# Optimization experiments

Measured on AMD Instinct MI355X. Metric: run time of the kernel, lower is better.

## Reference

```python
import jax, jax.numpy as jnp
import numpy as np
from jax import lax

B, C, H, W, K = 32, 128, 56, 56, 5
CR = C // 4          # reduced channels in weight-gen MLP
CE = 4 * C           # expanded channels
EPS = 1e-6


def setup_inputs() -> dict:
    key = jax.random.key(0)
    ks = jax.random.split(key, 8)
    s = lambda fan: 1.0 / np.sqrt(fan)
    return {
        "x": jax.random.normal(ks[0], (B, C, H, W), jnp.float32),
        "w_fc1": jax.random.normal(ks[1], (CR, C), jnp.float32) * s(C),
        "ln1_w": jnp.ones((CR,), jnp.float32),
        "ln1_b": jnp.zeros((CR,), jnp.float32),
        "w_fc2": jax.random.normal(ks[2], (C * K * K, CR), jnp.float32) * s(CR),
        "ln2_w": jnp.ones((C,), jnp.float32),
        "ln2_b": jnp.zeros((C,), jnp.float32),
        "w_expand": jax.random.normal(ks[3], (CE, C), jnp.float32) * s(C),
        "w_shrink": jax.random.normal(ks[4], (C, CE), jnp.float32) * s(CE),
        "grn_gamma": jax.random.normal(ks[5], (CE,), jnp.float32) * 0.1,
        "grn_beta": jax.random.normal(ks[6], (CE,), jnp.float32) * 0.1,
    }


def _ln(v, w, b, axis):
    u = v.mean(axis, keepdims=True)
    s2 = jnp.square(v - u).mean(axis, keepdims=True)
    return (v - u) * lax.rsqrt(s2 + EPS) * w + b


def reference(x, w_fc1, ln1_w, ln1_b, w_fc2, ln2_w, ln2_b, w_expand, w_shrink,
              grn_gamma, grn_beta):
    b, c, h, w = x.shape
    # ---- dynamic weight generation: pool -> fc1 -> LN -> fc2 ----
    pooled = x.mean((2, 3))                                  # [B, C]
    hdn = pooled @ w_fc1.T                                   # [B, CR]
    hdn = _ln(hdn, ln1_w, ln1_b, axis=-1)                    # channels_first LN over CR
    dyn = hdn @ w_fc2.T                                      # [B, C*K*K]
    dyn_w = dyn.reshape(b * c, 1, K, K)                      # per-sample depthwise kernels
    # ---- per-sample dynamic depthwise conv (groups = B*C) ----
    pad = K // 2
    out = lax.conv_general_dilated(
        x.reshape(1, b * c, h, w), dyn_w,
        window_strides=(1, 1), padding=[(pad, pad), (pad, pad)],
        dimension_numbers=("NCHW", "OIHW", "NCHW"),
        feature_group_count=b * c,
    ).reshape(b, c, h, w)
    # ---- LN (channels_first) over channel dim ----
    u = out.mean(1, keepdims=True)
    s2 = jnp.square(out - u).mean(1, keepdims=True)
    out = (out - u) * lax.rsqrt(s2 + EPS)
    out = ln2_w[None, :, None, None] * out + ln2_b[None, :, None, None]
    # ---- expand 1x1 -> GELU -> GRN -> shrink 1x1 ----
    out = jnp.einsum("bchw,oc->bohw", out, w_expand)         # [B, 4C, H, W]
    out = jax.nn.gelu(out, approximate=False)
    gx = jnp.sqrt(jnp.sum(jnp.square(out), axis=(2, 3), keepdims=True))  # [B,4C,1,1]
    nx = gx / (gx.mean(1, keepdims=True) + EPS)
    g = grn_gamma[None, :, None, None]
    bt = grn_beta[None, :, None, None]
    out = g * (out * nx) + bt + out
    out = jnp.einsum("bohw,co->bchw", out, w_shrink)         # [B, C, H, W]
    return out + x
```

## Files before the change

### kernel.cpp

```cpp
#include <hip/hip_runtime.h>
#include <hip/hip_bf16.h>

#define B_   32
#define C_   128
#define H_   56
#define W_   56
#define HW_  (H_*W_)
#define BHW_ (B_*HW_)
#define K5_  5
#define KK_  25
#define CR_  32
#define CE_  512
#define EPS_ 1e-6f

typedef __hip_bfloat16 bf16;
typedef __attribute__((ext_vector_type(8))) short short8;
typedef __attribute__((ext_vector_type(4))) float f32x4;


__device__ __forceinline__ float wave_reduce_sum(float v) {
#pragma unroll
  for (int off = 32; off > 0; off >>= 1) v += __shfl_down(v, off, 64);
  return v;
}
__device__ __forceinline__ float bf2f(unsigned short u) {
  return __uint_as_float(((unsigned)u) << 16);
}
__device__ __forceinline__ unsigned short f2bf_bits(float f) {
  bf16 h = __float2bfloat16(f);
  unsigned short u;
  __builtin_memcpy(&u, &h, 2);
  return u;
}
__device__ __forceinline__ float fast_gelu(float v) {
  float t = __expf(-1.702f * v);
  return v * __builtin_amdgcn_rcpf(1.0f + t);
}

__global__ __launch_bounds__(256) void prep_kernel(const float* __restrict__ we,
                                                   const float* __restrict__ ws,
                                                   bf16* __restrict__ weB,
                                                   bf16* __restrict__ wsB,
                                                   float* __restrict__ gx2) {
  int i = blockIdx.x * 256 + threadIdx.x;
  if (i < CE_ * C_)          weB[i] = __float2bfloat16(we[i]);
  else if (i < 2 * CE_ * C_) wsB[i - CE_ * C_] = __float2bfloat16(ws[i - CE_ * C_]);
  else                       gx2[i - 2 * CE_ * C_] = 0.f;
}

__global__ __launch_bounds__(256) void pool_kernel(const float* __restrict__ x,
                                                   float* __restrict__ pooled) {
  int bc = blockIdx.x;
  const float4* xp4 = reinterpret_cast<const float4*>(x + (size_t)bc * HW_);
  float s = 0.f;
  for (int i = threadIdx.x; i < 784; i += 256) {
    float4 v = xp4[i];
    s += (v.x + v.y) + (v.z + v.w);
  }
  s = wave_reduce_sum(s);
  __shared__ float red[4];
  int lane = threadIdx.x & 63, wid = threadIdx.x >> 6;
  if (lane == 0) red[wid] = s;
  __syncthreads();
  if (threadIdx.x == 0) pooled[bc] = (red[0] + red[1] + red[2] + red[3]) * (1.0f / HW_);
}

__global__ __launch_bounds__(256) void fc_kernel(const float* __restrict__ pooled,
                                                 const float* __restrict__ w_fc1,
                                                 const float* __restrict__ ln1_w,
                                                 const float* __restrict__ ln1_b,
                                                 const float* __restrict__ w_fc2,
                                                 float* __restrict__ dyn) {
  int b = blockIdx.x;
  int tid = threadIdx.x;
  __shared__ float sp[C_];
  __shared__ float sh[CR_];
  __shared__ float shn[CR_];
  __shared__ float stats[2];
  if (tid < C_) sp[tid] = pooled[b * C_ + tid];
  __syncthreads();
  if (tid < CR_) {
    float acc = 0.f;
    const float* wr = w_fc1 + tid * C_;
#pragma unroll 4
    for (int c = 0; c < C_; ++c) acc += sp[c] * wr[c];
    sh[tid] = acc;
  }
  __syncthreads();
  if (tid == 0) {
    float u = 0.f;
    for (int j = 0; j < CR_; ++j) u += sh[j];
    u *= (1.0f / CR_);
    float v = 0.f;
    for (int j = 0; j < CR_; ++j) { float d = sh[j] - u; v += d * d; }
    v *= (1.0f / CR_);
    stats[0] = u;
    stats[1] = rsqrtf(v + EPS_);
  }
  __syncthreads();
  if (tid < CR_) shn[tid] = (sh[tid] - stats[0]) * stats[1] * ln1_w[tid] + ln1_b[tid];
  __syncthreads();
  for (int i = tid; i < C_ * KK_; i += 256) {
    const float* wr = w_fc2 + i * CR_;
    float acc = 0.f;
#pragma unroll
    for (int j = 0; j < CR_; ++j) acc += shn[j] * wr[j];
    dyn[b * (C_ * KK_) + i] = acc;
  }
}

__global__ __launch_bounds__(256) void conv_kernel(const float* __restrict__ x,
                                                   const float* __restrict__ dyn,
                                                   bf16* __restrict__ z) {
  int bc = blockIdx.x;
  int b = bc >> 7;
  int c = bc & 127;
  int tid = threadIdx.x;
  __shared__ float xs[(H_ + 4) * 64];
  __shared__ float wks[KK_];
  {
    int r = tid >> 6;
    int rr = (r < 2) ? r : (56 + r);
    xs[rr * 64 + (tid & 63)] = 0.f;
  }
  if (tid < 224) {
    int r = tid >> 2, q = tid & 3;
    int col = (q < 2) ? q : (56 + q);
    xs[(r + 2) * 64 + col] = 0.f;
  }
  if (tid < KK_) wks[tid] = dyn[b * (C_ * KK_) + c * KK_ + tid];
  const float4* xp4 = reinterpret_cast<const float4*>(x + (size_t)bc * HW_);
  for (int i = tid; i < 784; i += 256) {
    float4 v = xp4[i];
    int h = i / 14, w4 = (i % 14) * 4;
    float* dst = &xs[(h + 2) * 64 + 2 + w4];
    dst[0] = v.x; dst[1] = v.y; dst[2] = v.z; dst[3] = v.w;
  }
  __syncthreads();
  float wr[KK_];
#pragma unroll
  for (int j = 0; j < KK_; ++j) wr[j] = wks[j];
  for (int g = tid; g < 784; g += 256) {
    int h = g / 14;
    int w4 = (g % 14) * 4;
    float a0 = 0.f, a1 = 0.f, a2 = 0.f, a3 = 0.f;
#pragma unroll
    for (int dh = 0; dh < K5_; ++dh) {
      const float* row = &xs[(h + dh) * 64 + w4];
      float4 va = *reinterpret_cast<const float4*>(row);
      float4 vb = *reinterpret_cast<const float4*>(row + 4);
      float v0 = va.x, v1 = va.y, v2 = va.z, v3 = va.w;
      float v4 = vb.x, v5 = vb.y, v6 = vb.z, v7 = vb.w;
      float u0 = wr[dh * 5 + 0], u1 = wr[dh * 5 + 1], u2 = wr[dh * 5 + 2];
      float u3 = wr[dh * 5 + 3], u4 = wr[dh * 5 + 4];
      a0 += v0 * u0 + v1 * u1 + v2 * u2 + v3 * u3 + v4 * u4;
      a1 += v1 * u0 + v2 * u1 + v3 * u2 + v4 * u3 + v5 * u4;
      a2 += v2 * u0 + v3 * u1 + v4 * u2 + v5 * u3 + v6 * u4;
      a3 += v3 * u0 + v4 * u1 + v5 * u2 + v6 * u3 + v7 * u4;
    }
    size_t base = (size_t)bc * HW_ + h * W_ + w4;
    ushort4 pk = make_ushort4(f2bf_bits(a0), f2bf_bits(a1), f2bf_bits(a2), f2bf_bits(a3));
    *reinterpret_cast<ushort4*>(reinterpret_cast<unsigned short*>(z) + base) = pk;
  }
}

__global__ __launch_bounds__(256) void ln_kernel(const bf16* __restrict__ z,
                                                 const float* __restrict__ ln2_w,
                                                 const float* __restrict__ ln2_b,
                                                 bf16* __restrict__ yT) {
  int hw0 = blockIdx.x * 64;
  int b = blockIdx.y;
  int tid = threadIdx.x;
  int wq = tid & 63;
  int cq = tid >> 6;
  __shared__ unsigned short zt[C_][64];
  __shared__ unsigned short yt[64][136];
  __shared__ float redS[4][64];
  __shared__ float redQ[4][64];
  __shared__ float meanArr[64];
  __shared__ float invArr[64];
  float s = 0.f, q = 0.f;
  const unsigned short* zp = reinterpret_cast<const unsigned short*>(z);
#pragma unroll 4
  for (int k = 0; k < 32; ++k) {
    int c = cq * 32 + k;
    unsigned short u = zp[((size_t)(b * C_ + c)) * HW_ + hw0 + wq];
    float v = bf2f(u);
    s += v;
    q += v * v;
    zt[c][wq] = u;
  }
  redS[cq][wq] = s;
  redQ[cq][wq] = q;
  __syncthreads();
  if (cq == 0) {
    float ss = redS[0][wq] + redS[1][wq] + redS[2][wq] + redS[3][wq];
    float qq = redQ[0][wq] + redQ[1][wq] + redQ[2][wq] + redQ[3][wq];
    float m = ss * (1.0f / C_);
    float var = qq * (1.0f / C_) - m * m;
    meanArr[wq] = m;
    invArr[wq] = rsqrtf(fmaxf(var, 0.f) + EPS_);
  }
  __syncthreads();
  float m = meanArr[wq], iv = invArr[wq];
#pragma unroll
  for (int g = 0; g < 4; ++g) {
    unsigned short pk[8];
#pragma unroll
    for (int i = 0; i < 8; ++i) {
      int c = cq * 32 + g * 8 + i;
      float v = bf2f(zt[c][wq]);
      pk[i] = f2bf_bits((v - m) * iv * ln2_w[c] + ln2_b[c]);
    }
    int4 t;
    __builtin_memcpy(&t, pk, 16);
    *reinterpret_cast<int4*>(&yt[wq][cq * 32 + g * 8]) = t;
  }
  __syncthreads();
  unsigned short* yp = reinterpret_cast<unsigned short*>(yT);
#pragma unroll
  for (int i = 0; i < 4; ++i) {
    int t = tid + 256 * i;
    int row = t >> 4, ch = t & 15;
    int4 v = *reinterpret_cast<const int4*>(&yt[row][ch * 8]);
    *reinterpret_cast<int4*>(yp + ((size_t)(b * HW_ + hw0 + row)) * C_ + ch * 8) = v;
  }
}

__global__ __launch_bounds__(256, 2) void expand_mfma(const bf16* __restrict__ yT,
                                                      const bf16* __restrict__ weB,
                                                      bf16* __restrict__ eT,
                                                      float* __restrict__ gx2) {
  int j0 = blockIdx.x * 128;
  int o0 = blockIdx.y * 128;
  int tid = threadIdx.x;
  int lane = tid & 63, wid = tid >> 6;
  int wm = wid >> 1, wn = wid & 1;
  int quad = lane >> 4, l15 = lane & 15;
  __shared__ __align__(16) char smem[2 * 128 * 136 * 2];
  short (*As)[136] = reinterpret_cast<short(*)[136]>(smem);
  short (*Bs)[136] = reinterpret_cast<short(*)[136]>(smem + 34816);
  const short* yS = reinterpret_cast<const short*>(yT);
  const short* weS = reinterpret_cast<const short*>(weB);
#pragma unroll
  for (int i = 0; i < 8; ++i) {
    int t = tid + 256 * i;
    int row = t >> 4, ch = t & 15;
    *reinterpret_cast<int4*>(&As[row][ch * 8]) =
        *reinterpret_cast<const int4*>(yS + (size_t)(j0 + row) * C_ + ch * 8);
    *reinterpret_cast<int4*>(&Bs[row][ch * 8]) =
        *reinterpret_cast<const int4*>(weS + (size_t)(o0 + row) * C_ + ch * 8);
  }
  __syncthreads();
  f32x4 acc[4][4] = {};
#pragma unroll
  for (int ks = 0; ks < 4; ++ks) {
    short8 a[4], b[4];
#pragma unroll
    for (int mf = 0; mf < 4; ++mf)
      a[mf] = *reinterpret_cast<const short8*>(&As[wm * 64 + mf * 16 + l15][ks * 32 + quad * 8]);
#pragma unroll
    for (int nf = 0; nf < 4; ++nf)
      b[nf] = *reinterpret_cast<const short8*>(&Bs[wn * 64 + nf * 16 + l15][ks * 32 + quad * 8]);
#pragma unroll
    for (int mf = 0; mf < 4; ++mf)
#pragma unroll
      for (int nf = 0; nf < 4; ++nf)
        acc[mf][nf] = __builtin_amdgcn_mfma_f32_16x16x32_bf16(a[mf], b[nf], acc[mf][nf], 0, 0, 0);
  }
  __syncthreads();
  short (*Es)[136] = reinterpret_cast<short(*)[136]>(smem);
#pragma unroll
  for (int mf = 0; mf < 4; ++mf) {
    int jm = j0 + wm * 64 + mf * 16;
    int bb = jm / HW_;
    int jrow = wm * 64 + mf * 16 + quad * 4;
#pragma unroll
    for (int nf = 0; nf < 4; ++nf) {
      int ocl = wn * 64 + nf * 16 + l15;
      float g2 = 0.f;
#pragma unroll
      for (int r = 0; r < 4; ++r) {
        float ge = fast_gelu(acc[mf][nf][r]);
        g2 += ge * ge;
        Es[jrow + r][ocl] = (short)f2bf_bits(ge);
      }
      g2 += __shfl_xor(g2, 16, 64);
      g2 += __shfl_xor(g2, 32, 64);
      if (quad == 0) atomicAdd(&gx2[bb * CE_ + o0 + ocl], g2);
    }
  }
  __syncthreads();
  unsigned short* eP = reinterpret_cast<unsigned short*>(eT);
#pragma unroll
  for (int i = 0; i < 8; ++i) {
    int t = tid + 256 * i;
    int row = t >> 4, ch = t & 15;
    int4 v = *reinterpret_cast<const int4*>(&Es[row][ch * 8]);
    *reinterpret_cast<int4*>(eP + (size_t)(j0 + row) * CE_ + o0 + ch * 8) = v;
  }
}

__global__ __launch_bounds__(512) void grn_scale_kernel(const float* __restrict__ gx2,
                                                        const float* __restrict__ gamma,
                                                        float* __restrict__ scale) {
  int b = blockIdx.x;
  int o = threadIdx.x;
  float gx = sqrtf(gx2[b * CE_ + o]);
  float s = wave_reduce_sum(gx);
  __shared__ float red[8];
  __shared__ float meansh;
  int lane = o & 63, wid = o >> 6;
  if (lane == 0) red[wid] = s;
  __syncthreads();
  if (o == 0) {
    float t = 0.f;
    for (int i = 0; i < 8; ++i) t += red[i];
    meansh = t * (1.0f / CE_);
  }
  __syncthreads();
  scale[b * CE_ + o] = 1.0f + gamma[o] * (gx / (meansh + EPS_));
}

__global__ __launch_bounds__(256) void sb_kernel(const float* __restrict__ w_shrink,
                                                 const float* __restrict__ beta,
                                                 float* __restrict__ sb) {
  int c = blockIdx.x;
  const float* wp = w_shrink + (size_t)c * CE_;
  float acc = 0.f;
  for (int o = threadIdx.x; o < CE_; o += 256) acc += wp[o] * beta[o];
  acc = wave_reduce_sum(acc);
  __shared__ float red[4];
  int lane = threadIdx.x & 63, wid = threadIdx.x >> 6;
  if (lane == 0) red[wid] = acc;
  __syncthreads();
  if (threadIdx.x == 0) sb[c] = red[0] + red[1] + red[2] + red[3];
}

__global__ __launch_bounds__(256, 2) void shrink_mfma(const bf16* __restrict__ eT,
                                                      const bf16* __restrict__ wsB,
                                                      const float* __restrict__ scale,
                                                      const float* __restrict__ sb,
                                                      const float* __restrict__ x,
                                                      float* __restrict__ out) {
  int hw0 = blockIdx.x * 128;
  int b = blockIdx.y;
  int tid = threadIdx.x;
  int lane = tid & 63, wid = tid >> 6;
  int wm = wid >> 1, wn = wid & 1;
  int quad = lane >> 4, l15 = lane & 15;
  __shared__ __align__(16) char smem[2 * 128 * 136 * 2];
  short (*As)[136] = reinterpret_cast<short(*)[136]>(smem);
  short (*Bs)[136] = reinterpret_cast<short(*)[136]>(smem + 34816);
  const short* eS  = reinterpret_cast<const short*>(eT) + (size_t)b * HW_ * CE_;
  const short* wsS = reinterpret_cast<const short*>(wsB);
  const float* scp = scale + b * CE_;
  f32x4 acc[4][4] = {};
#pragma unroll 1
  for (int kc = 0; kc < 4; ++kc) {
    int k0 = kc * 128;
#pragma unroll
    for (int i = 0; i < 8; ++i) {
      int t = tid + 256 * i;
      int row = t >> 4, ch = t & 15;
      int hwc = hw0 + row; if (hwc >= HW_) hwc = HW_ - 1;
      *reinterpret_cast<int4*>(&As[row][ch * 8]) =
          *reinterpret_cast<const int4*>(eS + (size_t)hwc * CE_ + k0 + ch * 8);
      int4 wv = *reinterpret_cast<const int4*>(wsS + (size_t)row * CE_ + k0 + ch * 8);
      float4 s0 = *reinterpret_cast<const float4*>(scp + k0 + ch * 8);
      float4 s1 = *reinterpret_cast<const float4*>(scp + k0 + ch * 8 + 4);
      unsigned short wu[8];
      __builtin_memcpy(wu, &wv, 16);
      unsigned short ru[8];
      ru[0] = f2bf_bits(bf2f(wu[0]) * s0.x);
      ru[1] = f2bf_bits(bf2f(wu[1]) * s0.y);
      ru[2] = f2bf_bits(bf2f(wu[2]) * s0.z);
      ru[3] = f2bf_bits(bf2f(wu[3]) * s0.w);
      ru[4] = f2bf_bits(bf2f(wu[4]) * s1.x);
      ru[5] = f2bf_bits(bf2f(wu[5]) * s1.y);
      ru[6] = f2bf_bits(bf2f(wu[6]) * s1.z);
      ru[7] = f2bf_bits(bf2f(wu[7]) * s1.w);
      int4 rv;
      __builtin_memcpy(&rv, ru, 16);
      *reinterpret_cast<int4*>(&Bs[row][ch * 8]) = rv;
    }
    __syncthreads();
#pragma unroll
    for (int ks = 0; ks < 4; ++ks) {
      short8 a[4], bfr[4];
#pragma unroll
      for (int mf = 0; mf < 4; ++mf)
        a[mf] = *reinterpret_cast<const short8*>(&As[wm * 64 + mf * 16 + l15][ks * 32 + quad * 8]);
#pragma unroll
      for (int nf = 0; nf < 4; ++nf)
        bfr[nf] = *reinterpret_cast<const short8*>(&Bs[wn * 64 + nf * 16 + l15][ks * 32 + quad * 8]);
#pragma unroll
      for (int mf = 0; mf < 4; ++mf)
#pragma unroll
        for (int nf = 0; nf < 4; ++nf)
          acc[mf][nf] = __builtin_amdgcn_mfma_f32_16x16x32_bf16(a[mf], bfr[nf], acc[mf][nf], 0, 0, 0);
    }
    __syncthreads();
  }
  float (*Ef)[133] = reinterpret_cast<float(*)[133]>(smem);
#pragma unroll
  for (int mf = 0; mf < 4; ++mf) {
    int hwr = wm * 64 + mf * 16 + quad * 4;
#pragma unroll
    for (int nf = 0; nf < 4; ++nf)
      *reinterpret_cast<f32x4*>(&Ef[wn * 64 + nf * 16 + l15][hwr]) = acc[mf][nf];
  }
  __syncthreads();
#pragma unroll
  for (int i = 0; i < 16; ++i) {
    int t = tid + 256 * i;
    int row = t >> 5, ch = t & 31;
    int hw = hw0 + ch * 4;
    if (hw < HW_) {
      size_t base = ((size_t)(b * C_ + row)) * HW_ + hw;
      float add = sb[row];
      f32x4 av = *reinterpret_cast<const f32x4*>(&Ef[row][ch * 4]);
      float4 xv = *reinterpret_cast<const float4*>(x + base);
      float4 ov;
      ov.x = av.x + add + xv.x;
      ov.y = av.y + add + xv.y;
      ov.z = av.z + add + xv.z;
      ov.w = av.w + add + xv.w;
      *reinterpret_cast<float4*>(out + base) = ov;
    }
  }
}

extern "C" void kernel_launch(void* const* d_in, const int* in_sizes, int n_in,
                              void* d_out, int out_size, void* d_ws, size_t ws_size,
                              hipStream_t stream) {
  (void)in_sizes; (void)n_in; (void)out_size; (void)ws_size;
  const float* x        = (const float*)d_in[0];
  const float* w_fc1    = (const float*)d_in[1];
  const float* ln1_w    = (const float*)d_in[2];
  const float* ln1_b    = (const float*)d_in[3];
  const float* w_fc2    = (const float*)d_in[4];
  const float* ln2_w    = (const float*)d_in[5];
  const float* ln2_b    = (const float*)d_in[6];
  const float* w_expand = (const float*)d_in[7];
  const float* w_shrink = (const float*)d_in[8];
  const float* gamma    = (const float*)d_in[9];
  const float* beta     = (const float*)d_in[10];
  float* out = (float*)d_out;

  char* ws = (char*)d_ws;
  float* pooled = (float*)(ws + 0);
  float* dyn    = (float*)(ws + 16384);
  float* gx2    = (float*)(ws + 425984);
  float* scale  = (float*)(ws + 491520);
  float* sb     = (float*)(ws + 557056);
  bf16*  weB    = (bf16*)(ws + 557568);
  bf16*  wsB    = (bf16*)(ws + 688640);
  bf16*  yT     = (bf16*)(ws + 819712);
  bf16*  eT     = (bf16*)(ws + 26509824);
  bf16*  z      = eT;

  prep_kernel<<<576, 256, 0, stream>>>(w_expand, w_shrink, weB, wsB, gx2);
  sb_kernel<<<C_, 256, 0, stream>>>(w_shrink, beta, sb);
  pool_kernel<<<B_ * C_, 256, 0, stream>>>(x, pooled);
  fc_kernel<<<B_, 256, 0, stream>>>(pooled, w_fc1, ln1_w, ln1_b, w_fc2, dyn);
  conv_kernel<<<B_ * C_, 256, 0, stream>>>(x, dyn, z);
  ln_kernel<<<dim3(49, B_), 256, 0, stream>>>(z, ln2_w, ln2_b, yT);
  expand_mfma<<<dim3(784, 4), 256, 0, stream>>>(yT, weB, eT, gx2);
  grn_scale_kernel<<<B_, 512, 0, stream>>>(gx2, gamma, scale);
  shrink_mfma<<<dim3(25, B_), 256, 0, stream>>>(eT, wsB, scale, sb, x, out);
}
```

Measured before the change: 273.3 us.

## Shrink LDS tiles in expand/shrink GEMMs to raise occupancy and swap grid order

```diff
diff --git a/kernel.cpp b/kernel.cpp
--- a/kernel.cpp
+++ b/kernel.cpp
@@ -227,49 +227,47 @@
   }
 }
 
-__global__ __launch_bounds__(256, 2) void expand_mfma(const bf16* __restrict__ yT,
+__global__ __launch_bounds__(256, 4) void expand_mfma(const bf16* __restrict__ yT,
                                                       const bf16* __restrict__ weB,
                                                       bf16* __restrict__ eT,
                                                       float* __restrict__ gx2) {
-  int j0 = blockIdx.x * 128;
-  int o0 = blockIdx.y * 128;
+  int o0 = blockIdx.x * 128;
+  int j0 = blockIdx.y * 128;
   int tid = threadIdx.x;
   int lane = tid & 63, wid = tid >> 6;
   int wm = wid >> 1, wn = wid & 1;
   int quad = lane >> 4, l15 = lane & 15;
-  __shared__ __align__(16) char smem[2 * 128 * 136 * 2];
-  short (*As)[136] = reinterpret_cast<short(*)[136]>(smem);
-  short (*Bs)[136] = reinterpret_cast<short(*)[136]>(smem + 34816);
-  const short* yS = reinterpret_cast<const short*>(yT);
+  __shared__ __align__(16) char smem[128 * 136 * 2];
+  short (*As)[40] = reinterpret_cast<short(*)[40]>(&smem[0]);
+  short (*Bs)[40] = reinterpret_cast<short(*)[40]>(&smem[10240]);
+  f32x4 acc[4][4] = {};
+  const short* yTs = reinterpret_cast<const short*>(yT);
   const short* weS = reinterpret_cast<const short*>(weB);
-#pragma unroll
-  for (int i = 0; i < 8; ++i) {
-    int t = tid + 256 * i;
-    int row = t >> 4, ch = t & 15;
-    *reinterpret_cast<int4*>(&As[row][ch * 8]) =
-        *reinterpret_cast<const int4*>(yS + (size_t)(j0 + row) * C_ + ch * 8);
-    *reinterpret_cast<int4*>(&Bs[row][ch * 8]) =
-        *reinterpret_cast<const int4*>(weS + (size_t)(o0 + row) * C_ + ch * 8);
-  }
-  __syncthreads();
-  f32x4 acc[4][4] = {};
-#pragma unroll
-  for (int ks = 0; ks < 4; ++ks) {
-    short8 a[4], b[4];
+  for (int k0 = 0; k0 < C_; k0 += 32) {
+#pragma unroll
+    for (int t = tid; t < 512; t += 256) {
+      int r = t >> 2, ch = t & 3;
+      int4 va = *reinterpret_cast<const int4*>(yTs + (size_t)(j0 + r) * C_ + k0 + ch * 8);
+      *reinterpret_cast<int4*>(&As[r][ch * 8]) = va;
+      int4 vb = *reinterpret_cast<const int4*>(weS + (size_t)(o0 + r) * C_ + k0 + ch * 8);
+      *reinterpret_cast<int4*>(&Bs[r][ch * 8]) = vb;
+    }
+    __syncthreads();
+    short8 a[4], bfr[4];
 #pragma unroll
     for (int mf = 0; mf < 4; ++mf)
-      a[mf] = *reinterpret_cast<const short8*>(&As[wm * 64 + mf * 16 + l15][ks * 32 + quad * 8]);
+      a[mf] = *reinterpret_cast<const short8*>(&As[wm * 64 + mf * 16 + l15][quad * 8]);
 #pragma unroll
     for (int nf = 0; nf < 4; ++nf)
-      b[nf] = *reinterpret_cast<const short8*>(&Bs[wn * 64 + nf * 16 + l15][ks * 32 + quad * 8]);
+      bfr[nf] = *reinterpret_cast<const short8*>(&Bs[wn * 64 + nf * 16 + l15][quad * 8]);
 #pragma unroll
     for (int mf = 0; mf < 4; ++mf)
 #pragma unroll
       for (int nf = 0; nf < 4; ++nf)
-        acc[mf][nf] = __builtin_amdgcn_mfma_f32_16x16x32_bf16(a[mf], b[nf], acc[mf][nf], 0, 0, 0);
-  }
-  __syncthreads();
-  short (*Es)[136] = reinterpret_cast<short(*)[136]>(smem);
+        acc[mf][nf] = __builtin_amdgcn_mfma_f32_16x16x32_bf16(a[mf], bfr[nf], acc[mf][nf], 0, 0, 0);
+    __syncthreads();
+  }
+  short (*Es)[136] = reinterpret_cast<short(*)[136]>(&smem[0]);
 #pragma unroll
   for (int mf = 0; mf < 4; ++mf) {
     int jm = j0 + wm * 64 + mf * 16;
@@ -277,17 +275,17 @@
     int jrow = wm * 64 + mf * 16 + quad * 4;
 #pragma unroll
     for (int nf = 0; nf < 4; ++nf) {
-      int ocl = wn * 64 + nf * 16 + l15;
+      int oc = wn * 64 + nf * 16 + l15;
       float g2 = 0.f;
 #pragma unroll
       for (int r = 0; r < 4; ++r) {
         float ge = fast_gelu(acc[mf][nf][r]);
         g2 += ge * ge;
-        Es[jrow + r][ocl] = (short)f2bf_bits(ge);
+        Es[jrow + r][oc] = (short)f2bf_bits(ge);
       }
       g2 += __shfl_xor(g2, 16, 64);
       g2 += __shfl_xor(g2, 32, 64);
-      if (quad == 0) atomicAdd(&gx2[bb * CE_ + o0 + ocl], g2);
+      if (quad == 0) atomicAdd(&gx2[bb * CE_ + o0 + oc], g2);
     }
   }
   __syncthreads();
@@ -337,7 +335,7 @@
   if (threadIdx.x == 0) sb[c] = red[0] + red[1] + red[2] + red[3];
 }
 
-__global__ __launch_bounds__(256, 2) void shrink_mfma(const bf16* __restrict__ eT,
+__global__ __launch_bounds__(256, 4) void shrink_mfma(const bf16* __restrict__ eT,
                                                       const bf16* __restrict__ wsB,
                                                       const float* __restrict__ scale,
                                                       const float* __restrict__ sb,
@@ -349,20 +347,20 @@
   int lane = tid & 63, wid = tid >> 6;
   int wm = wid >> 1, wn = wid & 1;
   int quad = lane >> 4, l15 = lane & 15;
-  __shared__ __align__(16) char smem[2 * 128 * 136 * 2];
-  short (*As)[136] = reinterpret_cast<short(*)[136]>(smem);
-  short (*Bs)[136] = reinterpret_cast<short(*)[136]>(smem + 34816);
+  __shared__ __align__(16) char smem[36864];
+  short (*As)[72] = reinterpret_cast<short(*)[72]>(&smem[0]);
+  short (*Bs)[72] = reinterpret_cast<short(*)[72]>(&smem[18432]);
   const short* eS  = reinterpret_cast<const short*>(eT) + (size_t)b * HW_ * CE_;
   const short* wsS = reinterpret_cast<const short*>(wsB);
   const float* scp = scale + b * CE_;
   f32x4 acc[4][4] = {};
 #pragma unroll 1
-  for (int kc = 0; kc < 4; ++kc) {
-    int k0 = kc * 128;
-#pragma unroll
-    for (int i = 0; i < 8; ++i) {
+  for (int kc = 0; kc < 8; ++kc) {
+    int k0 = kc * 64;
+#pragma unroll
+    for (int i = 0; i < 4; ++i) {
       int t = tid + 256 * i;
-      int row = t >> 4, ch = t & 15;
+      int row = t >> 3, ch = t & 7;
       int hwc = hw0 + row; if (hwc >= HW_) hwc = HW_ - 1;
       *reinterpret_cast<int4*>(&As[row][ch * 8]) =
           *reinterpret_cast<const int4*>(eS + (size_t)hwc * CE_ + k0 + ch * 8);
@@ -386,7 +384,7 @@
     }
     __syncthreads();
 #pragma unroll
-    for (int ks = 0; ks < 4; ++ks) {
+    for (int ks = 0; ks < 2; ++ks) {
       short8 a[4], bfr[4];
 #pragma unroll
       for (int mf = 0; mf < 4; ++mf)
@@ -402,32 +400,39 @@
     }
     __syncthreads();
   }
-  float (*Ef)[133] = reinterpret_cast<float(*)[133]>(smem);
-#pragma unroll
-  for (int mf = 0; mf < 4; ++mf) {
-    int hwr = wm * 64 + mf * 16 + quad * 4;
-#pragma unroll
-    for (int nf = 0; nf < 4; ++nf)
-      *reinterpret_cast<f32x4*>(&Ef[wn * 64 + nf * 16 + l15][hwr]) = acc[mf][nf];
-  }
-  __syncthreads();
-#pragma unroll
-  for (int i = 0; i < 16; ++i) {
-    int t = tid + 256 * i;
-    int row = t >> 5, ch = t & 31;
-    int hw = hw0 + ch * 4;
-    if (hw < HW_) {
-      size_t base = ((size_t)(b * C_ + row)) * HW_ + hw;
-      float add = sb[row];
-      f32x4 av = *reinterpret_cast<const f32x4*>(&Ef[row][ch * 4]);
-      float4 xv = *reinterpret_cast<const float4*>(x + base);
-      float4 ov;
-      ov.x = av.x + add + xv.x;
-      ov.y = av.y + add + xv.y;
-      ov.z = av.z + add + xv.z;
-      ov.w = av.w + add + xv.w;
-      *reinterpret_cast<float4*>(out + base) = ov;
-    }
+  float (*Ef)[132] = reinterpret_cast<float(*)[132]>(&smem[0]);
+#pragma unroll 1
+  for (int phase = 0; phase < 2; ++phase) {
+    if (wn == phase) {
+#pragma unroll
+      for (int mf = 0; mf < 4; ++mf) {
+        int hwr = wm * 64 + mf * 16 + quad * 4;
+#pragma unroll
+        for (int nf = 0; nf < 4; ++nf)
+          *reinterpret_cast<f32x4*>(&Ef[nf * 16 + l15][hwr]) = acc[mf][nf];
+      }
+    }
+    __syncthreads();
+#pragma unroll
+    for (int i = 0; i < 8; ++i) {
+      int t = tid + 256 * i;
+      int row = t >> 5, ch = t & 31;
+      int hw = hw0 + ch * 4;
+      if (hw < HW_) {
+        int c = phase * 64 + row;
+        size_t base = ((size_t)(b * C_ + c)) * HW_ + hw;
+        float add = sb[c];
+        f32x4 av = *reinterpret_cast<const f32x4*>(&Ef[row][ch * 4]);
+        float4 xv = *reinterpret_cast<const float4*>(x + base);
+        float4 ov;
+        ov.x = av.x + add + xv.x;
+        ov.y = av.y + add + xv.y;
+        ov.z = av.z + add + xv.z;
+        ov.w = av.w + add + xv.w;
+        *reinterpret_cast<float4*>(out + base) = ov;
+      }
+    }
+    __syncthreads();
   }
 }
 
@@ -466,7 +471,7 @@
   fc_kernel<<<B_, 256, 0, stream>>>(pooled, w_fc1, ln1_w, ln1_b, w_fc2, dyn);
   conv_kernel<<<B_ * C_, 256, 0, stream>>>(x, dyn, z);
   ln_kernel<<<dim3(49, B_), 256, 0, stream>>>(z, ln2_w, ln2_b, yT);
-  expand_mfma<<<dim3(784, 4), 256, 0, stream>>>(yT, weB, eT, gx2);
+  expand_mfma<<<dim3(4, 784), 256, 0, stream>>>(yT, weB, eT, gx2);
   grn_scale_kernel<<<B_, 512, 0, stream>>>(gx2, gamma, scale);
   shrink_mfma<<<dim3(25, B_), 256, 0, stream>>>(eT, wsB, scale, sb, x, out);
 }
```

Result: no change. 271.0 us (-0.8%).
